# Performance work log

Hardware: AMD Instinct MI355X
Metric: run time of the kernel (lower is better)

## Reference

```python
import jax, jax.numpy as jnp
import numpy as np
import math

ALPHA = 2.0  # spikingjelly surrogate.ATan default alpha
NB_STEPS, NUM_IN, NUM_HID, NUM_OUT = 100, 784, 100, 10
BATCH = 1024
TAU_LIF = 2.0

@jax.custom_vjp
def atan_spike(x):
    # Heaviside forward, ATan surrogate backward
    return (x >= 0.0).astype(x.dtype)

def _atan_fwd(x):
    return atan_spike(x), x

def _atan_bwd(x, g):
    return (g * (ALPHA / 2.0) / (1.0 + (jnp.pi / 2.0 * ALPHA * x) ** 2),)

atan_spike.defvjp(_atan_fwd, _atan_bwd)


def setup_inputs() -> dict:
    key = jax.random.key(0)
    ks = jax.random.split(key, 3)
    x = jax.random.normal(ks[0], (BATCH, NB_STEPS, NUM_IN), jnp.float32)
    tau_syn = 2.0
    # spikingjelly SynapseFilter(learnable=True): w init = -log(tau - 1)
    w_syn1 = jnp.asarray(-math.log(tau_syn - 1.0), jnp.float32)
    w_syn2 = jnp.asarray(-math.log(tau_syn - 1.0), jnp.float32)
    W1 = jax.random.normal(ks[1], (NUM_HID, NUM_IN), jnp.float32) / np.sqrt(NUM_IN).astype(np.float32)
    b1 = jnp.zeros((NUM_HID,), jnp.float32)
    W2 = jax.random.normal(ks[2], (NUM_OUT, NUM_HID), jnp.float32) / np.sqrt(NUM_HID).astype(np.float32)
    b2 = jnp.zeros((NUM_OUT,), jnp.float32)
    return dict(x=x, w_syn1=w_syn1, W1=W1, b1=b1, w_syn2=w_syn2, W2=W2, b2=b2)


def reference(x, w_syn1, W1, b1, w_syn2, W2, b2):
    B = x.shape[0]
    inv1 = jax.nn.sigmoid(w_syn1)  # 1/tau of filter 1
    inv2 = jax.nn.sigmoid(w_syn2)
    s1 = jnp.zeros((B, NUM_IN), x.dtype)
    v1 = jnp.zeros((B, NUM_HID), x.dtype)
    s2 = jnp.zeros((B, NUM_HID), x.dtype)
    v2 = jnp.zeros((B, NUM_OUT), x.dtype)

    def step(carry, xt):
        s1, v1, s2, v2 = carry
        # SynapseFilter 1: s = s - s*sigmoid(w) + in
        s1 = s1 - s1 * inv1 + xt
        h1 = s1 @ W1.T + b1
        # LIF 1: decay_input=True, v_reset=0: v += (x - (v - 0)) / tau
        v1 = v1 + (h1 - v1) / TAU_LIF
        sp1 = atan_spike(v1 - 1.0)       # v_threshold = 1.0
        v1 = v1 * (1.0 - sp1)            # hard reset to v_reset = 0
        # SynapseFilter 2
        s2 = s2 - s2 * inv2 + sp1
        h2 = s2 @ W2.T + b2
        # LIF 2: v_reset=None (soft reset), v_threshold=0, decay_input=True
        v2 = v2 + (h2 - v2) / TAU_LIF
        sp2 = atan_spike(v2 - 0.0)
        v2 = v2 - sp2 * 0.0              # soft reset subtracts spike*threshold (=0)
        return (s1, v1, s2, v2), None

    (s1, v1, s2, v2), _ = jax.lax.scan(step, (s1, v1, s2, v2), jnp.swapaxes(x, 0, 1))
    # Net.forward returns self.fc[-1].v: final membrane potential of last LIF
    return v2
```

## Files before the change

kernel.cpp:

```cpp
#include <hip/hip_runtime.h>
#include <math.h>


#define NSTEPS 100
#define NHID 100
#define KDIM 784
#define BKT 28
#define NOUT 10

typedef float v2f __attribute__((ext_vector_type(2)));

__global__ __launch_bounds__(256)
void wt_transpose(const float* __restrict__ W1, float* __restrict__ Wt) {
  const int idx = blockIdx.x * 256 + threadIdx.x;
  if (idx >= KDIM * 128) return;
  const int k = idx >> 7, s = idx & 127, cg = s >> 5, i = s & 31;
  const int j = 25 * cg + i;
  Wt[idx] = (i < 25) ? W1[(size_t)j * KDIM + k] : 0.0f;
}

__global__ __launch_bounds__(256, 2)
void snn_fused3(const float* __restrict__ X, const float* __restrict__ Wt,
                const float* __restrict__ wsyn1p, const float* __restrict__ b1,
                const float* __restrict__ wsyn2p, const float* __restrict__ W2,
                const float* __restrict__ b2, float* __restrict__ out) {
  __shared__ float Xs[BKT][256];
  __shared__ float Cs[2][25][106];
  __shared__ float zsh[2][NHID];

  const int tid = threadIdx.x;
  const int l   = tid & 63;
  const int cg  = __builtin_amdgcn_readfirstlane(tid >> 6);
  const long b0 = 2L * blockIdx.x;

  const int sb = tid >> 7;
  const int st = ((tid & 127) < NSTEPS) ? (tid & 127) : (NSTEPS - 1);
  const float* __restrict__ Xrow = X + ((b0 + sb) * NSTEPS + st) * (size_t)KDIM;

  v2f  acc2[4][12];
  float accs[4];
#pragma unroll
  for (int i = 0; i < 4; ++i) {
    accs[i] = 0.0f;
#pragma unroll
    for (int c = 0; c < 12; ++c) acc2[i][c] = (v2f){0.0f, 0.0f};
  }

  float4 pf[7];
#pragma unroll
  for (int q = 0; q < 7; ++q) pf[q] = *(const float4*)(Xrow + 4 * q);

  const float* __restrict__ wgrp = Wt + 32 * cg;

  for (int kt = 0; kt < KDIM; kt += BKT) {
    __syncthreads();
#pragma unroll
    for (int q = 0; q < 7; ++q) {
      Xs[4 * q + 0][tid] = pf[q].x;
      Xs[4 * q + 1][tid] = pf[q].y;
      Xs[4 * q + 2][tid] = pf[q].z;
      Xs[4 * q + 3][tid] = pf[q].w;
    }
    __syncthreads();
    if (kt + BKT < KDIM) {
      const float* xp = Xrow + kt + BKT;
#pragma unroll
      for (int q = 0; q < 7; ++q) pf[q] = *(const float4*)(xp + 4 * q);
    }

#pragma unroll 4
    for (int k = 0; k < BKT; ++k) {
      const float4 xv = *(const float4*)&Xs[k][4 * l];
      const float* __restrict__ wk = wgrp + (size_t)(kt + k) * 128;
      float w[26];
#pragma unroll
      for (int i2 = 0; i2 < 13; ++i2)
        *(v2f*)(w + 2 * i2) = *(const v2f*)(wk + 2 * i2);

      const v2f xd0 = {xv.x, xv.x};
      const v2f xd1 = {xv.y, xv.y};
      const v2f xd2 = {xv.z, xv.z};
      const v2f xd3 = {xv.w, xv.w};
#pragma unroll
      for (int c2 = 0; c2 < 12; ++c2) {
        const v2f wv = *(const v2f*)(w + 2 * c2);
        acc2[0][c2] = __builtin_elementwise_fma(xd0, wv, acc2[0][c2]);
        acc2[1][c2] = __builtin_elementwise_fma(xd1, wv, acc2[1][c2]);
        acc2[2][c2] = __builtin_elementwise_fma(xd2, wv, acc2[2][c2]);
        acc2[3][c2] = __builtin_elementwise_fma(xd3, wv, acc2[3][c2]);
      }
      const float w24 = w[24];
      accs[0] = fmaf(xv.x, w24, accs[0]);
      accs[1] = fmaf(xv.y, w24, accs[1]);
      accs[2] = fmaf(xv.z, w24, accs[2]);
      accs[3] = fmaf(xv.w, w24, accs[3]);
    }
  }

  const float inv1 = 1.f / (1.f + expf(-wsyn1p[0]));
  const float inv2 = 1.f / (1.f + expf(-wsyn2p[0]));
  const int sb2 = tid >> 7;
  const int j   = tid & 127;
  const float bj = (j < NHID) ? b1[j] : 0.f;
  float S = 0.f, v1 = 0.f, s2 = 0.f, z = 0.f;
  float at = 0x1p-100f;

  for (int q = 0; q < 4; ++q) {
    __syncthreads();
#pragma unroll
    for (int i = 0; i < 4; ++i) {
      const int r  = 4 * l + i;
      const int bb = r >> 7;
      const int t  = r & 127;
      const int tt = t - 25 * q;
      if (t < NSTEPS && tt >= 0 && tt < 25) {
        float* crow = &Cs[bb][tt][25 * cg];
#pragma unroll
        for (int c2 = 0; c2 < 12; ++c2) {
          crow[2 * c2 + 0] = acc2[i][c2].x;
          crow[2 * c2 + 1] = acc2[i][c2].y;
        }
        crow[24] = accs[i];
      }
    }
    __syncthreads();
    if (j < NHID) {
#pragma unroll
      for (int tt = 0; tt < 25; ++tt) {
        const float u = Cs[sb2][tt][j];
        S = S - S * inv1 + u;
        const float h = S + bj;
        v1 = v1 + (h - v1) * 0.5f;
        const float sp = (v1 >= 1.0f) ? 1.0f : 0.0f;
        v1 = v1 * (1.0f - sp);
        s2 = s2 - s2 * inv2 + sp;
        z  = fmaf(at, s2, z);
        at *= 2.0f;
      }
    }
  }

  if (j < NHID) zsh[sb2][j] = z;
  __syncthreads();

  if (tid < 2 * NOUT) {
    const int bb = tid / NOUT;
    const int jo = tid % NOUT;
    float a = b2[jo];
    const float* __restrict__ wrow = W2 + jo * NHID;
#pragma unroll
    for (int jj = 0; jj < NHID; ++jj) a = fmaf(zsh[bb][jj], wrow[jj], a);
    out[(b0 + bb) * NOUT + jo] = a;
  }
}

extern "C" void kernel_launch(void* const* d_in, const int* in_sizes, int n_in,
                              void* d_out, int out_size, void* d_ws, size_t ws_size,
                              hipStream_t stream) {
  const float* x     = (const float*)d_in[0];
  const float* wsyn1 = (const float*)d_in[1];
  const float* W1    = (const float*)d_in[2];
  const float* b1    = (const float*)d_in[3];
  const float* wsyn2 = (const float*)d_in[4];
  const float* W2    = (const float*)d_in[5];
  const float* b2    = (const float*)d_in[6];
  float* out = (float*)d_out;
  float* Wt  = (float*)d_ws;

  wt_transpose<<<dim3((KDIM * 128 + 255) / 256), dim3(256), 0, stream>>>(W1, Wt);
  snn_fused3<<<dim3(512), dim3(256), 0, stream>>>(x, Wt, wsyn1, b1, wsyn2, W2,
                                                  b2, out);
}
```

Before: 554.6 us.

## Process one sample per block with two rows per thread for higher occupancy

Each block now handles a single batch sample instead of two, with each thread accumulating two time-step rows instead of four. The K tile shrinks and launch bounds allow four blocks per CU, cutting register and LDS use to raise occupancy. In exchange, each loaded weight vector is reused across only two rows, doubling weight load traffic per FMA.

```diff
diff --git a/kernel.cpp b/kernel.cpp
--- a/kernel.cpp
+++ b/kernel.cpp
@@ -5,7 +5,8 @@
 #define NSTEPS 100
 #define NHID 100
 #define KDIM 784
-#define BKT 28
+#define BKT 16
+#define NROWS 128
 #define NOUT 10
 
 typedef float v2f __attribute__((ext_vector_type(2)));
@@ -19,58 +20,62 @@
   Wt[idx] = (i < 25) ? W1[(size_t)j * KDIM + k] : 0.0f;
 }
 
-__global__ __launch_bounds__(256, 2)
-void snn_fused3(const float* __restrict__ X, const float* __restrict__ Wt,
+__global__ __launch_bounds__(256, 4)
+void snn_fused4(const float* __restrict__ X, const float* __restrict__ Wt,
                 const float* __restrict__ wsyn1p, const float* __restrict__ b1,
                 const float* __restrict__ wsyn2p, const float* __restrict__ W2,
                 const float* __restrict__ b2, float* __restrict__ out) {
-  __shared__ float Xs[BKT][256];
-  __shared__ float Cs[2][25][106];
-  __shared__ float zsh[2][NHID];
+  __shared__ float Xs[BKT][NROWS];
+  __shared__ float Cs[25][106];
+  __shared__ float zsh[NHID];
 
   const int tid = threadIdx.x;
   const int l   = tid & 63;
   const int cg  = __builtin_amdgcn_readfirstlane(tid >> 6);
-  const long b0 = 2L * blockIdx.x;
+  const long b  = blockIdx.x;
 
-  const int sb = tid >> 7;
-  const int st = ((tid & 127) < NSTEPS) ? (tid & 127) : (NSTEPS - 1);
-  const float* __restrict__ Xrow = X + ((b0 + sb) * NSTEPS + st) * (size_t)KDIM;
+  const int row  = tid >> 1;
+  const int half = tid & 1;
+  const int st   = (row < NSTEPS) ? row : (NSTEPS - 1);
+  const float* __restrict__ Xrow =
+      X + ((size_t)b * NSTEPS + st) * KDIM + 8 * half;
 
-  v2f  acc2[4][12];
-  float accs[4];
+  v2f  acc2[2][12];
+  float accs[2];
 #pragma unroll
-  for (int i = 0; i < 4; ++i) {
+  for (int i = 0; i < 2; ++i) {
     accs[i] = 0.0f;
 #pragma unroll
     for (int c = 0; c < 12; ++c) acc2[i][c] = (v2f){0.0f, 0.0f};
   }
 
-  float4 pf[7];
-#pragma unroll
-  for (int q = 0; q < 7; ++q) pf[q] = *(const float4*)(Xrow + 4 * q);
+  float4 pf0 = *(const float4*)(Xrow);
+  float4 pf1 = *(const float4*)(Xrow + 4);
 
   const float* __restrict__ wgrp = Wt + 32 * cg;
 
   for (int kt = 0; kt < KDIM; kt += BKT) {
     __syncthreads();
-#pragma unroll
-    for (int q = 0; q < 7; ++q) {
-      Xs[4 * q + 0][tid] = pf[q].x;
-      Xs[4 * q + 1][tid] = pf[q].y;
-      Xs[4 * q + 2][tid] = pf[q].z;
-      Xs[4 * q + 3][tid] = pf[q].w;
+    {
+      const int k0 = 8 * half;
+      Xs[k0 + 0][row] = pf0.x;
+      Xs[k0 + 1][row] = pf0.y;
+      Xs[k0 + 2][row] = pf0.z;
+      Xs[k0 + 3][row] = pf0.w;
+      Xs[k0 + 4][row] = pf1.x;
+      Xs[k0 + 5][row] = pf1.y;
+      Xs[k0 + 6][row] = pf1.z;
+      Xs[k0 + 7][row] = pf1.w;
     }
     __syncthreads();
     if (kt + BKT < KDIM) {
-      const float* xp = Xrow + kt + BKT;
-#pragma unroll
-      for (int q = 0; q < 7; ++q) pf[q] = *(const float4*)(xp + 4 * q);
+      pf0 = *(const float4*)(Xrow + kt + BKT);
+      pf1 = *(const float4*)(Xrow + kt + BKT + 4);
     }
 
 #pragma unroll 4
     for (int k = 0; k < BKT; ++k) {
-      const float4 xv = *(const float4*)&Xs[k][4 * l];
+      const v2f xv = *(const v2f*)&Xs[k][2 * l];
       const float* __restrict__ wk = wgrp + (size_t)(kt + k) * 128;
       float w[26];
 #pragma unroll
@@ -79,42 +84,32 @@
 
       const v2f xd0 = {xv.x, xv.x};
       const v2f xd1 = {xv.y, xv.y};
-      const v2f xd2 = {xv.z, xv.z};
-      const v2f xd3 = {xv.w, xv.w};
 #pragma unroll
       for (int c2 = 0; c2 < 12; ++c2) {
         const v2f wv = *(const v2f*)(w + 2 * c2);
         acc2[0][c2] = __builtin_elementwise_fma(xd0, wv, acc2[0][c2]);
         acc2[1][c2] = __builtin_elementwise_fma(xd1, wv, acc2[1][c2]);
-        acc2[2][c2] = __builtin_elementwise_fma(xd2, wv, acc2[2][c2]);
-        acc2[3][c2] = __builtin_elementwise_fma(xd3, wv, acc2[3][c2]);
       }
       const float w24 = w[24];
       accs[0] = fmaf(xv.x, w24, accs[0]);
       accs[1] = fmaf(xv.y, w24, accs[1]);
-      accs[2] = fmaf(xv.z, w24, accs[2]);
-      accs[3] = fmaf(xv.w, w24, accs[3]);
     }
   }
 
   const float inv1 = 1.f / (1.f + expf(-wsyn1p[0]));
   const float inv2 = 1.f / (1.f + expf(-wsyn2p[0]));
-  const int sb2 = tid >> 7;
-  const int j   = tid & 127;
-  const float bj = (j < NHID) ? b1[j] : 0.f;
+  const float bj = (tid < NHID) ? b1[tid] : 0.f;
   float S = 0.f, v1 = 0.f, s2 = 0.f, z = 0.f;
   float at = 0x1p-100f;
 
   for (int q = 0; q < 4; ++q) {
     __syncthreads();
 #pragma unroll
-    for (int i = 0; i < 4; ++i) {
-      const int r  = 4 * l + i;
-      const int bb = r >> 7;
-      const int t  = r & 127;
-      const int tt = t - 25 * q;
-      if (t < NSTEPS && tt >= 0 && tt < 25) {
-        float* crow = &Cs[bb][tt][25 * cg];
+    for (int i = 0; i < 2; ++i) {
+      const int r  = 2 * l + i;
+      const int tt = r - 25 * q;
+      if (tt >= 0 && tt < 25 && r < NSTEPS) {
+        float* crow = &Cs[tt][25 * cg];
 #pragma unroll
         for (int c2 = 0; c2 < 12; ++c2) {
           crow[2 * c2 + 0] = acc2[i][c2].x;
@@ -124,10 +119,10 @@
       }
     }
     __syncthreads();
-    if (j < NHID) {
+    if (tid < NHID) {
 #pragma unroll
       for (int tt = 0; tt < 25; ++tt) {
-        const float u = Cs[sb2][tt][j];
+        const float u = Cs[tt][tid];
         S = S - S * inv1 + u;
         const float h = S + bj;
         v1 = v1 + (h - v1) * 0.5f;
@@ -140,17 +135,15 @@
     }
   }
 
-  if (j < NHID) zsh[sb2][j] = z;
+  if (tid < NHID) zsh[tid] = z;
   __syncthreads();
 
-  if (tid < 2 * NOUT) {
-    const int bb = tid / NOUT;
-    const int jo = tid % NOUT;
-    float a = b2[jo];
-    const float* __restrict__ wrow = W2 + jo * NHID;
+  if (tid < NOUT) {
+    float a = b2[tid];
+    const float* __restrict__ wrow = W2 + tid * NHID;
 #pragma unroll
-    for (int jj = 0; jj < NHID; ++jj) a = fmaf(zsh[bb][jj], wrow[jj], a);
-    out[(b0 + bb) * NOUT + jo] = a;
+    for (int jj = 0; jj < NHID; ++jj) a = fmaf(zsh[jj], wrow[jj], a);
+    out[b * NOUT + tid] = a;
   }
 }
 
@@ -168,6 +161,6 @@
   float* Wt  = (float*)d_ws;
 
   wt_transpose<<<dim3((KDIM * 128 + 255) / 256), dim3(256), 0, stream>>>(W1, Wt);
-  snn_fused3<<<dim3(512), dim3(256), 0, stream>>>(x, Wt, wsyn1, b1, wsyn2, W2,
-                                                  b2, out);
+  snn_fused4<<<dim3(1024), dim3(256), 0, stream>>>(x, Wt, wsyn1, b1, wsyn2, W2,
+                                                   b2, out);
 }
```

Measured after the change: 554.2 us. No clear change (-0.1%).
